# Performance work log

Hardware: AMD Instinct MI355X
Metric: run time of the kernel (lower is better)

## Reference

```python
import math
import jax, jax.numpy as jnp
import numpy as np

B, D = 64, 768
MAX_V, MAX_D, MAX_A, MAX_T = 512, 256, 128, 64
HEAD_SIZE = D // 12  # 64
SCALE = math.sqrt(HEAD_SIZE)


def make_pad_shifted_mask(input_mask, max_v, max_t, memory_len=0):
    # input_mask: (N, L) with L == memory_len + max_v + max_t
    N, L = input_mask.shape
    sm = jnp.zeros((max_v + max_t, L), input_mask.dtype)
    sm = sm.at[:, :memory_len + max_v].set(1.0)
    sm = sm.at[max_v:, memory_len + max_v:].set(
        jnp.tril(jnp.ones((max_t, max_t), input_mask.dtype)))
    return sm[None] * input_mask[:, None, :]  # (N, max_v+max_t, L)


def make_pad_shifted_mask_case2(mask, v1, v2, t):
    # mask: (N, v2 + t)
    sm = jnp.zeros((v1 + t, v2 + t), mask.dtype)
    sm = sm.at[:, :v2].set(1.0)
    sm = sm.at[v1:, v2:].set(jnp.tril(jnp.ones((t, t), mask.dtype)))
    return sm[None] * mask[:, None, :]  # (N, v1+t, v2+t)


def cross_attention(h1, h2, m1, m2, l1, l2):
    if l1 == l2:
        a12 = make_pad_shifted_mask(m2, l1, MAX_T)
        a21 = make_pad_shifted_mask(m1, l2, MAX_T)
    elif l1 > l2:
        a12 = make_pad_shifted_mask_case2(m2, l1, l2, MAX_T)
        a21 = make_pad_shifted_mask(m1, l2, MAX_T, l1 - l2)
    else:
        a12 = make_pad_shifted_mask(m2, l1, MAX_T, l2 - l1)
        a21 = make_pad_shifted_mask_case2(m1, l2, l1, MAX_T)
    a12 = (1.0 - a12) * -10000.0
    a21 = (1.0 - a21) * -10000.0
    s12 = jnp.einsum('bid,bjd->bij', h1, h2) / SCALE
    s21 = jnp.swapaxes(s12, -1, -2)
    p12 = jax.nn.softmax(s12 + a12, axis=-1)
    p21 = jax.nn.softmax(s21 + a21, axis=-1)
    c12 = jnp.einsum('bij,bjd->bid', p12, h2)
    c21 = jnp.einsum('bij,bjd->bid', p21, h1)
    return c12, c21


def setup_inputs() -> dict:
    key = jax.random.key(0)
    ks = jax.random.split(key, 9)
    Lv, Ld, La = MAX_V + MAX_T, MAX_D + MAX_T, MAX_A + MAX_T
    return {
        'video_embeddings': jax.random.normal(ks[0], (B, Lv, D), jnp.float32),
        'attention_mask': jnp.ones((B, Lv), jnp.float32),
        'detect_embeddings': jax.random.normal(ks[1], (B, Ld, D), jnp.float32),
        'attention_mask_det': jnp.ones((B, Ld), jnp.float32),
        'action_embeddings': jax.random.normal(ks[2], (B, La, D), jnp.float32),
        'attention_mask_act': jnp.ones((B, La), jnp.float32),
        'W_vid': jax.random.normal(ks[3], (D, D), jnp.float32) * 0.02,
        'b_vid': jnp.zeros((D,), jnp.float32),
        'W_det': jax.random.normal(ks[4], (D, D), jnp.float32) * 0.02,
        'b_det': jnp.zeros((D,), jnp.float32),
        'W_act': jax.random.normal(ks[5], (D, D), jnp.float32) * 0.02,
        'b_act': jnp.zeros((D,), jnp.float32),
    }


def reference(video_embeddings, attention_mask, detect_embeddings,
              attention_mask_det, action_embeddings, attention_mask_act,
              W_vid, b_vid, W_det, b_det, W_act, b_act):
    vid = video_embeddings @ W_vid.T + b_vid
    det = detect_embeddings @ W_det.T + b_det
    act = action_embeddings @ W_act.T + b_act
    c_vd, c_dv = cross_attention(vid, det, attention_mask, attention_mask_det, MAX_V, MAX_D)
    c_va, c_av = cross_attention(vid, act, attention_mask, attention_mask_act, MAX_V, MAX_A)
    c_ad, c_da = cross_attention(act, det, attention_mask_act, attention_mask_det, MAX_A, MAX_D)
    return (c_vd + c_va, c_dv + c_da, c_av + c_ad)
```

## Files before the change

### kernel.cpp

```cpp
#include <hip/hip_runtime.h>
#include <stdint.h>
#include <stddef.h>

typedef __attribute__((ext_vector_type(8))) short short8;
typedef __attribute__((ext_vector_type(4))) short short4v;
typedef __attribute__((ext_vector_type(4))) float floatx4;

__device__ __forceinline__ short f2bf(float f) {
    union { float f; uint32_t u; } v; v.f = f;
    uint32_t u = v.u + 0x7fffu + ((v.u >> 16) & 1u);
    return (short)(u >> 16);
}

__device__ __forceinline__ void async16(short* lds, const short* g) {
    __builtin_amdgcn_global_load_lds(
        (const __attribute__((address_space(1))) unsigned int*)g,
        (__attribute__((address_space(3))) unsigned int*)lds, 16, 0, 0);
}

__device__ __forceinline__ void stage128x32(short* lds, const short* src, size_t ld, int t) {
    const short* g = src + (size_t)(t >> 2) * ld + (t & 3) * 8;
    async16(lds + t * 8, g);
    async16(lds + 2048 + t * 8, g + 64 * ld);
}

__global__ __launch_bounds__(256) void cast_kernel(const float* __restrict__ src,
                                                   short* __restrict__ dst, int n4) {
    int i = blockIdx.x * blockDim.x + threadIdx.x;
    if (i < n4) {
        float4 v = ((const float4*)src)[i];
        short4v o;
        o.x = f2bf(v.x); o.y = f2bf(v.y); o.z = f2bf(v.z); o.w = f2bf(v.w);
        ((short4v*)dst)[i] = o;
    }
}

__global__ __launch_bounds__(256) void proj_gemm(
    const short* __restrict__ A, const short* __restrict__ W,
    const float* __restrict__ bias,
    short* __restrict__ Y, short* __restrict__ Yt, int L)
{
    __shared__ short As[4096], Bs[4096];
    const int t = threadIdx.x, w = t >> 6, l = t & 63;
    const int wr = (w >> 1) * 64, wc = (w & 1) * 64, lr = l & 15, lq = l >> 4;
    const size_t m0 = (size_t)blockIdx.x * 128;
    const int n0 = blockIdx.y * 128;
    const short* Ab = A + m0 * 768;
    const short* Bb = W + (size_t)n0 * 768;

    floatx4 acc[4][4];
#pragma unroll
    for (int i = 0; i < 4; ++i)
#pragma unroll
        for (int j = 0; j < 4; ++j) acc[i][j] = (floatx4){0.f, 0.f, 0.f, 0.f};

    for (int k0 = 0; k0 < 768; k0 += 32) {
        stage128x32(As, Ab + k0, 768, t);
        stage128x32(Bs, Bb + k0, 768, t);
        __syncthreads();
        short8 af[4], bf[4];
#pragma unroll
        for (int i = 0; i < 4; ++i) af[i] = *(const short8*)(As + (wr + i * 16 + lr) * 32 + lq * 8);
#pragma unroll
        for (int j = 0; j < 4; ++j) bf[j] = *(const short8*)(Bs + (wc + j * 16 + lr) * 32 + lq * 8);
#pragma unroll
        for (int i = 0; i < 4; ++i)
#pragma unroll
            for (int j = 0; j < 4; ++j)
                acc[i][j] = __builtin_amdgcn_mfma_f32_16x16x32_bf16(af[i], bf[j], acc[i][j], 0, 0, 0);
        __syncthreads();
    }

#pragma unroll
    for (int i = 0; i < 4; ++i) {
        const int mb = (int)m0 + wr + i * 16 + lq * 4;
        const int b_ = mb / L, pos = mb - b_ * L;
#pragma unroll
        for (int j = 0; j < 4; ++j) {
            const int n = n0 + wc + j * 16 + lr;
            const float bv = bias[n];
            short4v tv;
#pragma unroll
            for (int r2 = 0; r2 < 4; ++r2) {
                short hv = f2bf(acc[i][j][r2] + bv);
                Y[(size_t)(mb + r2) * 768 + n] = hv;
                tv[r2] = hv;
            }
            *(short4v*)(Yt + ((size_t)b_ * 768 + n) * L + pos) = tv;
        }
    }
}

__global__ __launch_bounds__(256) void s_gemm(
    const short* __restrict__ Q, const short* __restrict__ K,
    const float* __restrict__ mask, float* __restrict__ S, int R, int C)
{
    __shared__ short As[4096], Bs[4096];
    const int t = threadIdx.x, w = t >> 6, l = t & 63;
    const int wr = (w >> 1) * 64, wc = (w & 1) * 64, lr = l & 15, lq = l >> 4;
    const int b = blockIdx.z;
    const int m0 = blockIdx.x * 128, n0 = blockIdx.y * 128;
    const short* Ab = Q + ((size_t)b * R + m0) * 768;
    const short* Bb = K + ((size_t)b * C + n0) * 768;

    floatx4 acc[4][4];
#pragma unroll
    for (int i = 0; i < 4; ++i)
#pragma unroll
        for (int j = 0; j < 4; ++j) acc[i][j] = (floatx4){0.f, 0.f, 0.f, 0.f};

    for (int k0 = 0; k0 < 768; k0 += 32) {
        stage128x32(As, Ab + k0, 768, t);
        stage128x32(Bs, Bb + k0, 768, t);
        __syncthreads();
        short8 af[4], bf[4];
#pragma unroll
        for (int i = 0; i < 4; ++i) af[i] = *(const short8*)(As + (wr + i * 16 + lr) * 32 + lq * 8);
#pragma unroll
        for (int j = 0; j < 4; ++j) bf[j] = *(const short8*)(Bs + (wc + j * 16 + lr) * 32 + lq * 8);
#pragma unroll
        for (int i = 0; i < 4; ++i)
#pragma unroll
            for (int j = 0; j < 4; ++j)
                acc[i][j] = __builtin_amdgcn_mfma_f32_16x16x32_bf16(af[i], bf[j], acc[i][j], 0, 0, 0);
        __syncthreads();
    }

    const int Rm = R - 64, Cm = C - 64;
#pragma unroll
    for (int j = 0; j < 4; ++j) {
        const int n = n0 + wc + j * 16 + lr;
        if (n >= C) continue;
        const float mv = mask[(size_t)b * C + n];
#pragma unroll
        for (int i = 0; i < 4; ++i) {
            const int mb = m0 + wr + i * 16 + lq * 4;
#pragma unroll
            for (int r2 = 0; r2 < 4; ++r2) {
                const int mm = mb + r2;
                if (mm < R) {
                    const bool allowed = (n < Cm) || ((mm >= Rm) && ((n - Cm) <= (mm - Rm)));
                    const float am = allowed ? mv : 0.f;
                    S[((size_t)b * R + mm) * C + n] = acc[i][j][r2] * 0.125f + (am - 1.f) * 10000.f;
                }
            }
        }
    }
}

__global__ __launch_bounds__(256) void softmax_k(const float* __restrict__ S,
                                                 short* __restrict__ P, int C) {
    const int row = blockIdx.x * 4 + (threadIdx.x >> 6);
    const int l = threadIdx.x & 63;
    const float* s = S + (size_t)row * C;
    float v[9];
    int cnt = 0;
    float mx = -3.0e38f;
    for (int j = l; j < C; j += 64) { float x = s[j]; v[cnt++] = x; mx = fmaxf(mx, x); }
#pragma unroll
    for (int d = 32; d; d >>= 1) mx = fmaxf(mx, __shfl_xor(mx, d, 64));
    float sum = 0.f;
    for (int i = 0; i < cnt; ++i) { v[i] = __expf(v[i] - mx); sum += v[i]; }
#pragma unroll
    for (int d = 32; d; d >>= 1) sum += __shfl_xor(sum, d, 64);
    const float inv = 1.f / sum;
    short* p = P + (size_t)row * C;
    cnt = 0;
    for (int j = l; j < C; j += 64) p[j] = f2bf(v[cnt++] * inv);
}

__global__ __launch_bounds__(256) void pv_gemm(
    const short* __restrict__ P0, const short* __restrict__ Vt0, int C0,
    const short* __restrict__ P1, const short* __restrict__ Vt1, int C1,
    float* __restrict__ O, int R)
{
    __shared__ short As[4096], Bs[4096];
    const int t = threadIdx.x, w = t >> 6, l = t & 63;
    const int wr = (w >> 1) * 64, wc = (w & 1) * 64, lr = l & 15, lq = l >> 4;
    const int b = blockIdx.z;
    const int m0 = blockIdx.x * 128, n0 = blockIdx.y * 128;

    floatx4 acc[4][4];
#pragma unroll
    for (int i = 0; i < 4; ++i)
#pragma unroll
        for (int j = 0; j < 4; ++j) acc[i][j] = (floatx4){0.f, 0.f, 0.f, 0.f};

    for (int s = 0; s < 2; ++s) {
        const short* Ab = (s ? P1 : P0);
        const short* Bb = (s ? Vt1 : Vt0);
        const int C = s ? C1 : C0;
        Ab += ((size_t)b * R + m0) * C;
        Bb += ((size_t)b * 768 + n0) * C;
        for (int k0 = 0; k0 < C; k0 += 32) {
            stage128x32(As, Ab + k0, C, t);
            stage128x32(Bs, Bb + k0, C, t);
            __syncthreads();
            short8 af[4], bf[4];
#pragma unroll
            for (int i = 0; i < 4; ++i) af[i] = *(const short8*)(As + (wr + i * 16 + lr) * 32 + lq * 8);
#pragma unroll
            for (int j = 0; j < 4; ++j) bf[j] = *(const short8*)(Bs + (wc + j * 16 + lr) * 32 + lq * 8);
#pragma unroll
            for (int i = 0; i < 4; ++i)
#pragma unroll
                for (int j = 0; j < 4; ++j)
                    acc[i][j] = __builtin_amdgcn_mfma_f32_16x16x32_bf16(af[i], bf[j], acc[i][j], 0, 0, 0);
            __syncthreads();
        }
    }

#pragma unroll
    for (int i = 0; i < 4; ++i) {
        const int mb = m0 + wr + i * 16 + lq * 4;
#pragma unroll
        for (int j = 0; j < 4; ++j) {
            const int n = n0 + wc + j * 16 + lr;
#pragma unroll
            for (int r2 = 0; r2 < 4; ++r2) {
                if (mb + r2 < R)
                    O[((size_t)b * R + mb + r2) * 768 + n] = acc[i][j][r2];
            }
        }
    }
}

extern "C" void kernel_launch(void* const* d_in, const int* in_sizes, int n_in,
                              void* d_out, int out_size, void* d_ws, size_t ws_size,
                              hipStream_t stream) {
    const float* vidX = (const float*)d_in[0];
    const float* mV   = (const float*)d_in[1];
    const float* detX = (const float*)d_in[2];
    const float* mD   = (const float*)d_in[3];
    const float* actX = (const float*)d_in[4];
    const float* mA   = (const float*)d_in[5];
    const float* Wv   = (const float*)d_in[6];
    const float* bv   = (const float*)d_in[7];
    const float* Wd   = (const float*)d_in[8];
    const float* bd   = (const float*)d_in[9];
    const float* Wa   = (const float*)d_in[10];
    const float* ba   = (const float*)d_in[11];

    const size_t EV = 28311552, ED = 15728640, EA = 9437184;
    char* p = (char*)d_ws;
    auto alloc = [&](size_t bytes) { char* r = p; p += (bytes + 255) & ~255ULL; return r; };

    short* Wvb = (short*)alloc(589824 * 2);
    short* Wdb = (short*)alloc(589824 * 2);
    short* Wab = (short*)alloc(589824 * 2);
    short* Yv  = (short*)alloc(EV * 2);
    short* Yd  = (short*)alloc(ED * 2);
    short* Ya  = (short*)alloc(EA * 2);
    short* Ytv = (short*)alloc(EV * 2);
    short* Ytd = (short*)alloc(ED * 2);
    short* Yta = (short*)alloc(EA * 2);
    char* xs  = alloc((EV + ED + EA) * 2);
    short* Xv = (short*)xs;
    short* Xd = Xv + EV;
    short* Xa = Xd + ED;
    float* Sb = (float*)xs;
    short* Pvd = (short*)alloc((size_t)64 * 576 * 320 * 2);
    short* Pva = (short*)alloc((size_t)64 * 576 * 192 * 2);
    short* Pdv = (short*)alloc((size_t)64 * 320 * 576 * 2);
    short* Pda = (short*)alloc((size_t)64 * 320 * 192 * 2);
    short* Pav = (short*)alloc((size_t)64 * 192 * 576 * 2);
    short* Pad = (short*)alloc((size_t)64 * 192 * 320 * 2);
    (void)alloc(262144);

    float* o0 = (float*)d_out;
    float* o1 = o0 + EV;
    float* o2 = o1 + ED;

    cast_kernel<<<576, 256, 0, stream>>>(Wv, Wvb, 147456);
    cast_kernel<<<576, 256, 0, stream>>>(Wd, Wdb, 147456);
    cast_kernel<<<576, 256, 0, stream>>>(Wa, Wab, 147456);
    cast_kernel<<<27648, 256, 0, stream>>>(vidX, Xv, (int)(EV / 4));
    cast_kernel<<<15360, 256, 0, stream>>>(detX, Xd, (int)(ED / 4));
    cast_kernel<<<9216, 256, 0, stream>>>(actX, Xa, (int)(EA / 4));

    proj_gemm<<<dim3(288, 6), 256, 0, stream>>>(Xv, Wvb, bv, Yv, Ytv, 576);
    proj_gemm<<<dim3(160, 6), 256, 0, stream>>>(Xd, Wdb, bd, Yd, Ytd, 320);
    proj_gemm<<<dim3(96, 6), 256, 0, stream>>>(Xa, Wab, ba, Ya, Yta, 192);

    auto pair = [&](const short* Q, const short* K, const float* msk, short* Pout, int R, int C) {
        s_gemm<<<dim3((R + 127) / 128, (C + 127) / 128, 64), 256, 0, stream>>>(Q, K, msk, Sb, R, C);
        softmax_k<<<64 * R / 4, 256, 0, stream>>>(Sb, Pout, C);
    };
    pair(Yv, Yd, mD, Pvd, 576, 320);
    pair(Yv, Ya, mA, Pva, 576, 192);
    pair(Yd, Yv, mV, Pdv, 320, 576);
    pair(Yd, Ya, mA, Pda, 320, 192);
    pair(Ya, Yv, mV, Pav, 192, 576);
    pair(Ya, Yd, mD, Pad, 192, 320);

    pv_gemm<<<dim3(5, 6, 64), 256, 0, stream>>>(Pvd, Ytd, 320, Pva, Yta, 192, o0, 576);
    pv_gemm<<<dim3(3, 6, 64), 256, 0, stream>>>(Pdv, Ytv, 576, Pda, Yta, 192, o1, 320);
    pv_gemm<<<dim3(2, 6, 64), 256, 0, stream>>>(Pav, Ytv, 576, Pad, Ytd, 320, o2, 192);
}
```

Measured before the change: 1.249 ms.

## Fuse score GEMM, masking and softmax into one full-row kernel per key set

Replaces the separate score GEMM, which wrote fp32 scores to a scratch buffer, and the row softmax kernel with a templated kernel. Each 512-thread block computes a 64-row strip against all C keys, applies the mask, and does the row softmax in registers with cross-wave LDS reductions before writing bf16 probabilities. The six pair launches become three by grouping the two query sets that share a key set. This removes the fp32 score round trip through global memory and about nine launches. In exchange, large LDS tiles for C=576 and many accumulators per thread may reduce occupancy, and the K tile is re-staged for every 64-row strip.

```diff
diff --git a/kernel.cpp b/kernel.cpp
--- a/kernel.cpp
+++ b/kernel.cpp
@@ -91,82 +91,150 @@
     }
 }
 
-__global__ __launch_bounds__(256) void s_gemm(
-    const short* __restrict__ Q, const short* __restrict__ K,
-    const float* __restrict__ mask, float* __restrict__ S, int R, int C)
+template<int C>
+__global__ __launch_bounds__(512) void fused_sp(
+    const short* __restrict__ K,
+    const float* __restrict__ mask,
+    const short* __restrict__ Q0, int R0, short* __restrict__ P0,
+    const short* __restrict__ Q1, int R1, short* __restrict__ P1)
 {
-    __shared__ short As[4096], Bs[4096];
+    constexpr int NT = C / 16;
+    constexpr int NTW = NT / 4;
+    __shared__ short Ks[C * 32];
+    __shared__ short Qs[64 * 32];
+    __shared__ float red[4][64];
+
     const int t = threadIdx.x, w = t >> 6, l = t & 63;
-    const int wr = (w >> 1) * 64, wc = (w & 1) * 64, lr = l & 15, lq = l >> 4;
-    const int b = blockIdx.z;
-    const int m0 = blockIdx.x * 128, n0 = blockIdx.y * 128;
-    const short* Ab = Q + ((size_t)b * R + m0) * 768;
-    const short* Bb = K + ((size_t)b * C + n0) * 768;
-
-    floatx4 acc[4][4];
-#pragma unroll
-    for (int i = 0; i < 4; ++i)
-#pragma unroll
-        for (int j = 0; j < 4; ++j) acc[i][j] = (floatx4){0.f, 0.f, 0.f, 0.f};
+    const int wr2 = w >> 2;
+    const int wc  = w & 3;
+    const int lr = l & 15, lq = l >> 4;
+
+    const int b  = blockIdx.z;
+    const int pr = blockIdx.y;
+    const int R  = pr ? R1 : R0;
+    const int m0 = blockIdx.x * 64;
+    if (m0 >= R) return;
+
+    const short* Qb = (pr ? Q1 : Q0) + ((size_t)b * R + m0) * 768;
+    short*       Pb = (pr ? P1 : P0) + ((size_t)b * R + m0) * C;
+    const short* Kb = K + (size_t)b * C * 768;
+
+    floatx4 acc[2][NTW];
+#pragma unroll
+    for (int i = 0; i < 2; ++i)
+#pragma unroll
+        for (int j = 0; j < NTW; ++j) acc[i][j] = (floatx4){0.f, 0.f, 0.f, 0.f};
 
     for (int k0 = 0; k0 < 768; k0 += 32) {
-        stage128x32(As, Ab + k0, 768, t);
-        stage128x32(Bs, Bb + k0, 768, t);
+        constexpr int CH = C * 4;
+        for (int c = t; c < CH; c += 512)
+            async16(Ks + c * 8, Kb + (size_t)(c >> 2) * 768 + k0 + (c & 3) * 8);
+        if (t < 256)
+            async16(Qs + t * 8, Qb + (size_t)(t >> 2) * 768 + k0 + (t & 3) * 8);
         __syncthreads();
-        short8 af[4], bf[4];
-#pragma unroll
-        for (int i = 0; i < 4; ++i) af[i] = *(const short8*)(As + (wr + i * 16 + lr) * 32 + lq * 8);
-#pragma unroll
-        for (int j = 0; j < 4; ++j) bf[j] = *(const short8*)(Bs + (wc + j * 16 + lr) * 32 + lq * 8);
-#pragma unroll
-        for (int i = 0; i < 4; ++i)
-#pragma unroll
-            for (int j = 0; j < 4; ++j)
+
+        short8 af[2], bf[NTW];
+#pragma unroll
+        for (int i = 0; i < 2; ++i)
+            af[i] = *(const short8*)(Qs + (wr2 * 32 + i * 16 + lr) * 32 + lq * 8);
+#pragma unroll
+        for (int j = 0; j < NTW; ++j)
+            bf[j] = *(const short8*)(Ks + ((wc * NTW + j) * 16 + lr) * 32 + lq * 8);
+#pragma unroll
+        for (int i = 0; i < 2; ++i)
+#pragma unroll
+            for (int j = 0; j < NTW; ++j)
                 acc[i][j] = __builtin_amdgcn_mfma_f32_16x16x32_bf16(af[i], bf[j], acc[i][j], 0, 0, 0);
         __syncthreads();
     }
 
     const int Rm = R - 64, Cm = C - 64;
-#pragma unroll
-    for (int j = 0; j < 4; ++j) {
-        const int n = n0 + wc + j * 16 + lr;
-        if (n >= C) continue;
-        const float mv = mask[(size_t)b * C + n];
-#pragma unroll
-        for (int i = 0; i < 4; ++i) {
-            const int mb = m0 + wr + i * 16 + lq * 4;
+    float mval[NTW];
+#pragma unroll
+    for (int j = 0; j < NTW; ++j)
+        mval[j] = mask[(size_t)b * C + (wc * NTW + j) * 16 + lr];
+
+#pragma unroll
+    for (int i = 0; i < 2; ++i) {
+        const int mmb = m0 + wr2 * 32 + i * 16 + lq * 4;
+#pragma unroll
+        for (int j = 0; j < NTW; ++j) {
+            const int n = (wc * NTW + j) * 16 + lr;
 #pragma unroll
             for (int r2 = 0; r2 < 4; ++r2) {
-                const int mm = mb + r2;
-                if (mm < R) {
-                    const bool allowed = (n < Cm) || ((mm >= Rm) && ((n - Cm) <= (mm - Rm)));
-                    const float am = allowed ? mv : 0.f;
-                    S[((size_t)b * R + mm) * C + n] = acc[i][j][r2] * 0.125f + (am - 1.f) * 10000.f;
-                }
+                const int mm = mmb + r2;
+                const bool allowed = (n < Cm) || ((mm >= Rm) && ((n - Cm) <= (mm - Rm)));
+                const float am = allowed ? mval[j] : 0.f;
+                acc[i][j][r2] = acc[i][j][r2] * 0.125f + (am - 1.f) * 10000.f;
             }
         }
     }
-}
-
-__global__ __launch_bounds__(256) void softmax_k(const float* __restrict__ S,
-                                                 short* __restrict__ P, int C) {
-    const int row = blockIdx.x * 4 + (threadIdx.x >> 6);
-    const int l = threadIdx.x & 63;
-    const float* s = S + (size_t)row * C;
-    float v[9];
-    int cnt = 0;
-    float mx = -3.0e38f;
-    for (int j = l; j < C; j += 64) { float x = s[j]; v[cnt++] = x; mx = fmaxf(mx, x); }
-#pragma unroll
-    for (int d = 32; d; d >>= 1) mx = fmaxf(mx, __shfl_xor(mx, d, 64));
-    float sum = 0.f;
-    for (int i = 0; i < cnt; ++i) { v[i] = __expf(v[i] - mx); sum += v[i]; }
-#pragma unroll
-    for (int d = 32; d; d >>= 1) sum += __shfl_xor(sum, d, 64);
-    const float inv = 1.f / sum;
-    short* p = P + (size_t)row * C;
-    cnt = 0;
-    for (int j = l; j < C; j += 64) p[j] = f2bf(v[cnt++] * inv);
+
+    float pmax[2][4];
+#pragma unroll
+    for (int i = 0; i < 2; ++i)
+#pragma unroll
+        for (int r2 = 0; r2 < 4; ++r2) {
+            float m_ = -3.0e38f;
+#pragma unroll
+            for (int j = 0; j < NTW; ++j) m_ = fmaxf(m_, acc[i][j][r2]);
+#pragma unroll
+            for (int d = 1; d < 16; d <<= 1) m_ = fmaxf(m_, __shfl_xor(m_, d, 64));
+            pmax[i][r2] = m_;
+        }
+    if (lr == 0) {
+#pragma unroll
+        for (int i = 0; i < 2; ++i)
+#pragma unroll
+            for (int r2 = 0; r2 < 4; ++r2)
+                red[wc][wr2 * 32 + i * 16 + lq * 4 + r2] = pmax[i][r2];
+    }
+    __syncthreads();
+#pragma unroll
+    for (int i = 0; i < 2; ++i)
+#pragma unroll
+        for (int r2 = 0; r2 < 4; ++r2) {
+            const int rr = wr2 * 32 + i * 16 + lq * 4 + r2;
+            pmax[i][r2] = fmaxf(fmaxf(red[0][rr], red[1][rr]), fmaxf(red[2][rr], red[3][rr]));
+        }
+    __syncthreads();
+
+    float psum[2][4];
+#pragma unroll
+    for (int i = 0; i < 2; ++i)
+#pragma unroll
+        for (int r2 = 0; r2 < 4; ++r2) {
+            float s_ = 0.f;
+#pragma unroll
+            for (int j = 0; j < NTW; ++j) {
+                const float e = __expf(acc[i][j][r2] - pmax[i][r2]);
+                acc[i][j][r2] = e;
+                s_ += e;
+            }
+#pragma unroll
+            for (int d = 1; d < 16; d <<= 1) s_ += __shfl_xor(s_, d, 64);
+            psum[i][r2] = s_;
+        }
+    if (lr == 0) {
+#pragma unroll
+        for (int i = 0; i < 2; ++i)
+#pragma unroll
+            for (int r2 = 0; r2 < 4; ++r2)
+                red[wc][wr2 * 32 + i * 16 + lq * 4 + r2] = psum[i][r2];
+    }
+    __syncthreads();
+
+#pragma unroll
+    for (int i = 0; i < 2; ++i)
+#pragma unroll
+        for (int r2 = 0; r2 < 4; ++r2) {
+            const int rr = wr2 * 32 + i * 16 + lq * 4 + r2;
+            const float inv = 1.f / (red[0][rr] + red[1][rr] + red[2][rr] + red[3][rr]);
+            short* prow = Pb + (size_t)rr * C;
+#pragma unroll
+            for (int j = 0; j < NTW; ++j)
+                prow[(wc * NTW + j) * 16 + lr] = f2bf(acc[i][j][r2] * inv);
+        }
 }
 
 __global__ __launch_bounds__(256) void pv_gemm(
@@ -258,7 +326,6 @@
     short* Xv = (short*)xs;
     short* Xd = Xv + EV;
     short* Xa = Xd + ED;
-    float* Sb = (float*)xs;
     short* Pvd = (short*)alloc((size_t)64 * 576 * 320 * 2);
     short* Pva = (short*)alloc((size_t)64 * 576 * 192 * 2);
     short* Pdv = (short*)alloc((size_t)64 * 320 * 576 * 2);
@@ -282,16 +349,9 @@
     proj_gemm<<<dim3(160, 6), 256, 0, stream>>>(Xd, Wdb, bd, Yd, Ytd, 320);
     proj_gemm<<<dim3(96, 6), 256, 0, stream>>>(Xa, Wab, ba, Ya, Yta, 192);
 
-    auto pair = [&](const short* Q, const short* K, const float* msk, short* Pout, int R, int C) {
-        s_gemm<<<dim3((R + 127) / 128, (C + 127) / 128, 64), 256, 0, stream>>>(Q, K, msk, Sb, R, C);
-        softmax_k<<<64 * R / 4, 256, 0, stream>>>(Sb, Pout, C);
-    };
-    pair(Yv, Yd, mD, Pvd, 576, 320);
-    pair(Yv, Ya, mA, Pva, 576, 192);
-    pair(Yd, Yv, mV, Pdv, 320, 576);
-    pair(Yd, Ya, mA, Pda, 320, 192);
-    pair(Ya, Yv, mV, Pav, 192, 576);
-    pair(Ya, Yd, mD, Pad, 192, 320);
+    fused_sp<576><<<dim3(5, 2, 64), 512, 0, stream>>>(Yv, mV, Yd, 320, Pdv, Ya, 192, Pav);
+    fused_sp<320><<<dim3(9, 2, 64), 512, 0, stream>>>(Yd, mD, Yv, 576, Pvd, Ya, 192, Pad);
+    fused_sp<192><<<dim3(9, 2, 64), 512, 0, stream>>>(Ya, mA, Yv, 576, Pva, Yd, 320, Pda);
 
     pv_gemm<<<dim3(5, 6, 64), 256, 0, stream>>>(Pvd, Ytd, 320, Pva, Yta, 192, o0, 576);
     pv_gemm<<<dim3(3, 6, 64), 256, 0, stream>>>(Pdv, Ytv, 576, Pda, Yta, 192, o1, 320);
```

New measurement: 1.080 ms. 13.5% less time.
